# Optimization experiments

Measured on AMD Instinct MI355X. Metric: run time of the kernel, lower is better.

Reference implementation:

```python
import jax, jax.numpy as jnp
import numpy as np

EMBED = 256
HEADS = 8
LEVELS = 1
POINTS = 4
HEAD_DIM = EMBED // HEADS  # 32
SPATIAL = [(200, 200)]     # static (H, W) per level
BS = 2
NQ = 40000
NV = sum(h * w for h, w in SPATIAL)


def setup_inputs() -> dict:
    key = jax.random.key(0)
    ks = jax.random.split(key, 12)
    s = 0.02
    inp = {
        "query": jax.random.normal(ks[0], (BS, NQ, EMBED), jnp.float32),
        "value": jax.random.normal(ks[1], (BS, NV, EMBED), jnp.float32),
        "reference_points": jax.random.uniform(ks[2], (BS, NQ, LEVELS, 2), jnp.float32),
        "spatial_shapes": jnp.array(SPATIAL, dtype=jnp.int32),
        "W_value": jax.random.normal(ks[3], (EMBED, EMBED), jnp.float32) * s,
        "b_value": jax.random.normal(ks[4], (EMBED,), jnp.float32) * s,
        "W_off": jax.random.normal(ks[5], (EMBED, HEADS * LEVELS * POINTS * 2), jnp.float32) * s,
        "b_off": jax.random.normal(ks[6], (HEADS * LEVELS * POINTS * 2,), jnp.float32) * s,
        "W_attn": jax.random.normal(ks[7], (EMBED, HEADS * LEVELS * POINTS), jnp.float32) * s,
        "b_attn": jax.random.normal(ks[8], (HEADS * LEVELS * POINTS,), jnp.float32) * s,
        "W_out": jax.random.normal(ks[9], (EMBED, EMBED), jnp.float32) * s,
        "b_out": jax.random.normal(ks[10], (EMBED,), jnp.float32) * s,
    }
    return inp


def _bilinear_sample(v_l, x, y, H, W):
    """grid_sample(bilinear, padding zeros, align_corners=False) on flat spatial.
    v_l: [bs, heads, H*W, d]; x, y: [bs, nq, heads, P] pixel coords.
    Returns [bs, nq, heads, P, d]."""
    bs = v_l.shape[0]
    nq = x.shape[1]
    x0 = jnp.floor(x)
    y0 = jnp.floor(y)
    out = jnp.zeros((bs, nq, HEADS, POINTS, HEAD_DIM), v_l.dtype)
    for dx in (0, 1):
        for dy in (0, 1):
            xi = x0 + dx
            yi = y0 + dy
            w = (1.0 - jnp.abs(x - xi)) * (1.0 - jnp.abs(y - yi))
            valid = (xi >= 0) & (xi <= W - 1) & (yi >= 0) & (yi <= H - 1)
            xi_c = jnp.clip(xi, 0, W - 1).astype(jnp.int32)
            yi_c = jnp.clip(yi, 0, H - 1).astype(jnp.int32)
            idx = yi_c * W + xi_c                               # [bs,nq,heads,P]
            idx = idx.transpose(0, 2, 1, 3).reshape(bs, HEADS, nq * POINTS)
            g = jnp.take_along_axis(v_l, idx[..., None], axis=2)  # [bs,heads,nq*P,d]
            g = g.reshape(bs, HEADS, nq, POINTS, HEAD_DIM).transpose(0, 2, 1, 3, 4)
            out = out + g * (w * valid.astype(w.dtype))[..., None]
    return out


def reference(query, value, reference_points, spatial_shapes,
              W_value, b_value, W_off, b_off, W_attn, b_attn, W_out, b_out):
    bs, nq, _ = query.shape
    # value projection
    v = (value @ W_value + b_value).reshape(bs, -1, HEADS, HEAD_DIM)
    v = v.transpose(0, 2, 1, 3)  # [bs, heads, nv, d]
    # sampling offsets and attention weights from query
    off = (query @ W_off + b_off).reshape(bs, nq, HEADS, LEVELS, POINTS, 2)
    aw = (query @ W_attn + b_attn).reshape(bs, nq, HEADS, LEVELS * POINTS)
    aw = jax.nn.softmax(aw, axis=-1).reshape(bs, nq, HEADS, LEVELS, POINTS)
    # sampling locations in [0,1] (reference_points last dim == 2 branch)
    normalizer = jnp.stack([spatial_shapes[:, 1], spatial_shapes[:, 0]], -1).astype(query.dtype)  # [L,2]=(W,H)
    loc = reference_points[:, :, None, :, None, :] + off / normalizer[None, None, None, :, None, :]
    out = jnp.zeros((bs, nq, HEADS, HEAD_DIM), query.dtype)
    start = 0
    for lvl, (H, W) in enumerate(SPATIAL):
        v_l = v[:, :, start:start + H * W]            # [bs,heads,HW,d]
        g = 2.0 * loc[:, :, :, lvl] - 1.0             # [bs,nq,heads,P,2] in [-1,1]
        px = ((g[..., 0] + 1.0) * W - 1.0) / 2.0      # align_corners=False
        py = ((g[..., 1] + 1.0) * H - 1.0) / 2.0
        sampled = _bilinear_sample(v_l, px, py, H, W)  # [bs,nq,heads,P,d]
        out = out + (sampled * aw[:, :, :, lvl, :, None]).sum(axis=3)
        start += H * W
    out = out.reshape(bs, nq, EMBED) @ W_out + b_out
    # dropout is identity in eval; identity residual = query (no query_pos)
    return out + query
```

## Files before the change

### kernel.cpp

```cpp
#include <hip/hip_runtime.h>


typedef float  f4  __attribute__((ext_vector_type(4)));
typedef float  fx4 __attribute__((ext_vector_type(4)));
typedef short  s8  __attribute__((ext_vector_type(8)));
typedef short  s4  __attribute__((ext_vector_type(4)));
typedef int    i4  __attribute__((ext_vector_type(4)));
typedef unsigned int u4 __attribute__((ext_vector_type(4)));

#define KDIM    256
#define NVPIX   40000
#define GH      200
#define GW      200
#define LDP     68

__device__ __forceinline__ short f2bf(float f) {
  union { float f; unsigned u; } v; v.f = f;
  unsigned r = v.u + 0x7fffu + ((v.u >> 16) & 1u);
  return (short)(r >> 16);
}
__device__ __forceinline__ float bf2f(unsigned short h) {
  union { unsigned u; float f; } v; v.u = ((unsigned)h) << 16; return v.f;
}
__device__ __forceinline__ float asf(unsigned u) {
  union { unsigned u; float f; } v; v.u = u; return v.f;
}

__global__ void prep_k(const float* __restrict__ Wv, const float* __restrict__ Wo,
                       const float* __restrict__ Woff, const float* __restrict__ Wattn,
                       const float* __restrict__ boff, const float* __restrict__ battn,
                       unsigned short* __restrict__ Wv_t, unsigned short* __restrict__ Wo_t,
                       unsigned short* __restrict__ Wp_t, float* __restrict__ bp)
{
  int i = blockIdx.x * 256 + threadIdx.x;
  if (i < 65536) {
    int n = i >> 8, k = i & 255;
    Wv_t[i] = (unsigned short)f2bf(Wv[k * 256 + n]);
  } else if (i < 131072) {
    int j = i - 65536; int n = j >> 8, k = j & 255;
    Wo_t[j] = (unsigned short)f2bf(Wo[k * 256 + n]);
  } else if (i < 163840) {
    int j = i - 131072; int n = j >> 8, k = j & 255;
    float val = (n < 64) ? Woff[k * 64 + n] : ((n < 96) ? Wattn[k * 32 + (n - 64)] : 0.f);
    Wp_t[j] = (unsigned short)f2bf(val);
  } else if (i < 163968) {
    int j = i - 163840;
    bp[j] = (j < 64) ? boff[j] : ((j < 96) ? battn[j - 64] : 0.f);
  }
}

template<int ABF, int CBF, int RES, int BN>
__global__ __launch_bounds__(512)
void gemm_k(const void* __restrict__ Ap, const unsigned short* __restrict__ Bt,
            const float* __restrict__ bias, const float* __restrict__ resid,
            void* __restrict__ Cp)
{
  constexpr int ACCJ = BN / 64;
  constexpr int WN   = BN / 4;
  __shared__ short As[128 * LDP];
  __shared__ short Bs[BN * LDP];
  const int t  = threadIdx.x;
  const int m0 = blockIdx.x * 128;
  const int lane = t & 63;
  const int w  = t >> 6;
  const int wm = (w >> 2) * 64;
  const int wn = (w & 3) * WN;
  const int fr = lane & 15;
  const int quad = lane >> 4;

  fx4 acc[4][ACCJ];
  #pragma unroll
  for (int i = 0; i < 4; i++)
    #pragma unroll
    for (int j = 0; j < ACCJ; j++) { fx4 z = {0.f, 0.f, 0.f, 0.f}; acc[i][j] = z; }

  f4 pa[4];
  s8 pa8[2];
  s8 pb[ACCJ];

  auto loadA = [&](int k0) {
    if (ABF) {
      const unsigned short* base = (const unsigned short*)Ap + (size_t)m0 * KDIM + k0;
      #pragma unroll
      for (int j = 0; j < 2; j++) {
        int id = t + j * 512;
        int row = id >> 3, kp = (id & 7) * 8;
        pa8[j] = *(const s8*)(base + (size_t)row * KDIM + kp);
      }
    } else {
      const float* base = (const float*)Ap + (size_t)m0 * KDIM + k0;
      #pragma unroll
      for (int j = 0; j < 4; j++) {
        int id = t + j * 512;
        int row = id >> 4, kp = (id & 15) * 4;
        pa[j] = *(const f4*)(base + (size_t)row * KDIM + kp);
      }
    }
  };
  auto loadB = [&](int k0) {
    const unsigned short* base = Bt + k0;
    #pragma unroll
    for (int j = 0; j < ACCJ; j++) {
      int id = t + j * 512;
      int row = id >> 3, kp = (id & 7) * 8;
      pb[j] = *(const s8*)(base + (size_t)row * KDIM + kp);
    }
  };
  auto storeAB = [&]() {
    if (ABF) {
      #pragma unroll
      for (int j = 0; j < 2; j++) {
        int id = t + j * 512;
        int row = id >> 3, kp = (id & 7) * 8;
        *(s8*)(&As[row * LDP + kp]) = pa8[j];
      }
    } else {
      #pragma unroll
      for (int j = 0; j < 4; j++) {
        int id = t + j * 512;
        int row = id >> 4, kp = (id & 15) * 4;
        s4 c;
        #pragma unroll
        for (int e = 0; e < 4; e++) c[e] = f2bf(pa[j][e]);
        *(s4*)(&As[row * LDP + kp]) = c;
      }
    }
    #pragma unroll
    for (int j = 0; j < ACCJ; j++) {
      int id = t + j * 512;
      int row = id >> 3, kp = (id & 7) * 8;
      *(s8*)(&Bs[row * LDP + kp]) = pb[j];
    }
  };

  loadA(0); loadB(0);
  #pragma unroll
  for (int it = 0; it < 4; ++it) {
    __syncthreads();
    storeAB();
    __syncthreads();
    if (it < 3) { loadA((it + 1) * 64); loadB((it + 1) * 64); }
    #pragma unroll
    for (int kk = 0; kk < 2; kk++) {
      s8 afr[4], bfr[ACCJ];
      #pragma unroll
      for (int i = 0; i < 4; i++)
        afr[i] = *(const s8*)(&As[(wm + i * 16 + fr) * LDP + kk * 32 + quad * 8]);
      #pragma unroll
      for (int j = 0; j < ACCJ; j++)
        bfr[j] = *(const s8*)(&Bs[(wn + j * 16 + fr) * LDP + kk * 32 + quad * 8]);
      #pragma unroll
      for (int i = 0; i < 4; i++)
        #pragma unroll
        for (int j = 0; j < ACCJ; j++)
          acc[i][j] = __builtin_amdgcn_mfma_f32_16x16x32_bf16(afr[i], bfr[j], acc[i][j], 0, 0, 0);
    }
  }

  #pragma unroll
  for (int i = 0; i < 4; i++) {
    const int mbase = m0 + wm + i * 16 + quad * 4;
    #pragma unroll
    for (int j = 0; j < ACCJ; j++) {
      const int n = wn + j * 16 + fr;
      const float bn = bias[n];
      #pragma unroll
      for (int r = 0; r < 4; r++) {
        const size_t m = (size_t)(mbase + r);
        float v = acc[i][j][r] + bn;
        if (RES) v += resid[m * (size_t)BN + n];
        if (CBF) ((unsigned short*)Cp)[m * (size_t)BN + n] = (unsigned short)f2bf(v);
        else     ((float*)Cp)[m * (size_t)BN + n] = v;
      }
    }
  }
}

__global__ __launch_bounds__(256, 4)
void sample_k(const unsigned short* __restrict__ v, const float* __restrict__ p,
              const float* __restrict__ ref, unsigned short* __restrict__ o)
{
  const int t  = threadIdx.x;
  const int q0 = blockIdx.x * 8;
  __shared__ float sp[8][128];
  __shared__ float sref[16];
  __shared__ float sw[8][8][4][4];
  __shared__ int   so[8][8][4][4];
  {
    const float* pb = p + (size_t)q0 * 128;
    float* spf = &sp[0][0];
    *(f4*)(spf + t * 4) = *(const f4*)(pb + t * 4);
    if (t < 16) sref[t] = ref[(size_t)q0 * 2 + t];
  }
  __syncthreads();

  {
    const int qa = t >> 5;
    const int ha = (t >> 2) & 7;
    const int pa_ = t & 3;
    const float lg0 = sp[qa][64 + ha * 4 + 0], lg1 = sp[qa][64 + ha * 4 + 1];
    const float lg2 = sp[qa][64 + ha * 4 + 2], lg3 = sp[qa][64 + ha * 4 + 3];
    const float mx = fmaxf(fmaxf(lg0, lg1), fmaxf(lg2, lg3));
    const float e0 = __expf(lg0 - mx), e1 = __expf(lg1 - mx);
    const float e2 = __expf(lg2 - mx), e3 = __expf(lg3 - mx);
    const float inv = 1.f / (e0 + e1 + e2 + e3);
    const float a = ((pa_ == 0) ? e0 : (pa_ == 1) ? e1 : (pa_ == 2) ? e2 : e3) * inv;
    const float rx = sref[qa * 2], ry = sref[qa * 2 + 1];
    const float ox = sp[qa][ha * 8 + pa_ * 2], oy = sp[qa][ha * 8 + pa_ * 2 + 1];
    const float px = rx * 200.f + ox - 0.5f;
    const float py = ry * 200.f + oy - 0.5f;
    const float x0f = floorf(px), y0f = floorf(py);
    const int ix = (int)x0f, iy = (int)y0f;
    const float fx = px - x0f, fy = py - y0f;
    const float vx0 = (ix >= 0 && ix < GW) ? 1.f : 0.f;
    const float vx1 = (ix + 1 >= 0 && ix + 1 < GW) ? 1.f : 0.f;
    const float vy0 = (iy >= 0 && iy < GH) ? 1.f : 0.f;
    const float vy1 = (iy + 1 >= 0 && iy + 1 < GH) ? 1.f : 0.f;
    f4 wv;
    wv[0] = a * (1.f - fx) * (1.f - fy) * vx0 * vy0;
    wv[1] = a * fx * (1.f - fy) * vx1 * vy0;
    wv[2] = a * (1.f - fx) * fy * vx0 * vy1;
    wv[3] = a * fx * fy * vx1 * vy1;
    const int ix0c = min(max(ix, 0), GW - 1);
    const int ix1c = min(max(ix + 1, 0), GW - 1);
    const int iy0c = min(max(iy, 0), GH - 1);
    const int iy1c = min(max(iy + 1, 0), GH - 1);
    const int r0 = iy0c * (GW * 256);
    const int r1 = iy1c * (GW * 256);
    i4 ov;
    ov[0] = r0 + ix0c * 256;
    ov[1] = r0 + ix1c * 256;
    ov[2] = r1 + ix0c * 256;
    ov[3] = r1 + ix1c * 256;
    *(f4*)&sw[qa][ha][pa_][0] = wv;
    *(i4*)&so[qa][ha][pa_][0] = ov;
  }
  __syncthreads();

  const int qi = t >> 5;
  const int h  = (t >> 2) & 7;
  const int dg = t & 3;
  const int q  = q0 + qi;
  const unsigned short* vb = v + ((q0 >= 40000) ? (size_t)NVPIX * 256 : 0);
  const int cbase = h * 32 + dg * 8;

  i4 ofs[4];
  #pragma unroll
  for (int pt = 0; pt < 4; pt++) ofs[pt] = *(const i4*)&so[qi][h][pt][0];

  u4 g[16];
  #pragma unroll
  for (int pt = 0; pt < 4; pt++)
    #pragma unroll
    for (int c = 0; c < 4; c++)
      g[pt * 4 + c] = *(const u4*)(vb + (unsigned)(ofs[pt][c] + cbase));

  f4 wts[4];
  #pragma unroll
  for (int pt = 0; pt < 4; pt++) wts[pt] = *(const f4*)&sw[qi][h][pt][0];

  float acc[8];
  #pragma unroll
  for (int e = 0; e < 8; e++) acc[e] = 0.f;

  #pragma unroll
  for (int pt = 0; pt < 4; pt++) {
    #pragma unroll
    for (int c = 0; c < 4; c++) {
      const float wk = wts[pt][c];
      const u4 gu = g[pt * 4 + c];
      #pragma unroll
      for (int d = 0; d < 4; d++) {
        const unsigned u = gu[d];
        acc[2 * d]     += wk * asf(u << 16);
        acc[2 * d + 1] += wk * asf(u & 0xffff0000u);
      }
    }
  }

  s8 res;
  #pragma unroll
  for (int e = 0; e < 8; e++) res[e] = f2bf(acc[e]);
  *(s8*)(o + (size_t)q * 256 + cbase) = res;
}

extern "C" void kernel_launch(void* const* d_in, const int* in_sizes, int n_in,
                              void* d_out, int out_size, void* d_ws, size_t ws_size,
                              hipStream_t stream)
{
  const float* query = (const float*)d_in[0];
  const float* value = (const float*)d_in[1];
  const float* refp  = (const float*)d_in[2];
  const float* Wv    = (const float*)d_in[4];
  const float* bv    = (const float*)d_in[5];
  const float* Woff  = (const float*)d_in[6];
  const float* boff  = (const float*)d_in[7];
  const float* Wattn = (const float*)d_in[8];
  const float* battn = (const float*)d_in[9];
  const float* Wo    = (const float*)d_in[10];
  const float* bo    = (const float*)d_in[11];

  char* ws = (char*)d_ws;
  unsigned short* ws_v = (unsigned short*)ws;
  float*          ws_p = (float*)(ws + 40960000);
  unsigned short* ws_o = (unsigned short*)(ws + 81920000);
  unsigned short* Wv_t = (unsigned short*)(ws + 122880000);
  unsigned short* Wo_t = Wv_t + 65536;
  unsigned short* Wp_t = Wo_t + 65536;
  float*          bp   = (float*)(Wp_t + 32768);

  hipLaunchKernelGGL(prep_k, dim3(641), dim3(256), 0, stream,
                     Wv, Wo, Woff, Wattn, boff, battn, Wv_t, Wo_t, Wp_t, bp);
  hipLaunchKernelGGL((gemm_k<0, 1, 0, 256>), dim3(625), dim3(512), 0, stream,
                     (const void*)value, Wv_t, bv, (const float*)nullptr, (void*)ws_v);
  hipLaunchKernelGGL((gemm_k<0, 0, 0, 128>), dim3(625), dim3(512), 0, stream,
                     (const void*)query, Wp_t, bp, (const float*)nullptr, (void*)ws_p);
  hipLaunchKernelGGL(sample_k, dim3(10000), dim3(256), 0, stream,
                     ws_v, ws_p, refp, ws_o);
  hipLaunchKernelGGL((gemm_k<1, 0, 1, 256>), dim3(625), dim3(512), 0, stream,
                     (const void*)ws_o, Wo_t, bo, query, (void*)d_out);
}
```

Baseline: 341.4 us.

## Double-buffer GEMM shared tiles with two-deep register prefetch and lighter barriers

Measured after the change: 328.6 us. 3.7% less time.

```diff
diff --git a/kernel.cpp b/kernel.cpp
--- a/kernel.cpp
+++ b/kernel.cpp
@@ -57,8 +57,8 @@
 {
   constexpr int ACCJ = BN / 64;
   constexpr int WN   = BN / 4;
-  __shared__ short As[128 * LDP];
-  __shared__ short Bs[BN * LDP];
+  __shared__ short As[2][128 * LDP];
+  __shared__ short Bs[2][BN * LDP];
   const int t  = threadIdx.x;
   const int m0 = blockIdx.x * 128;
   const int lane = t & 63;
@@ -74,88 +74,94 @@
     #pragma unroll
     for (int j = 0; j < ACCJ; j++) { fx4 z = {0.f, 0.f, 0.f, 0.f}; acc[i][j] = z; }
 
-  f4 pa[4];
-  s8 pa8[2];
-  s8 pb[ACCJ];
-
-  auto loadA = [&](int k0) {
+  f4 paf[2][4];
+  s8 pab[2][2];
+  s8 pb [2][ACCJ];
+
+  auto loadT = [&](int k0, int s) {
     if (ABF) {
       const unsigned short* base = (const unsigned short*)Ap + (size_t)m0 * KDIM + k0;
       #pragma unroll
       for (int j = 0; j < 2; j++) {
         int id = t + j * 512;
-        int row = id >> 3, kp = (id & 7) * 8;
-        pa8[j] = *(const s8*)(base + (size_t)row * KDIM + kp);
+        pab[s][j] = *(const s8*)(base + (size_t)(id >> 3) * KDIM + (id & 7) * 8);
       }
     } else {
       const float* base = (const float*)Ap + (size_t)m0 * KDIM + k0;
       #pragma unroll
       for (int j = 0; j < 4; j++) {
         int id = t + j * 512;
-        int row = id >> 4, kp = (id & 15) * 4;
-        pa[j] = *(const f4*)(base + (size_t)row * KDIM + kp);
-      }
-    }
-  };
-  auto loadB = [&](int k0) {
-    const unsigned short* base = Bt + k0;
+        paf[s][j] = *(const f4*)(base + (size_t)(id >> 4) * KDIM + (id & 15) * 4);
+      }
+    }
+    const unsigned short* bbase = Bt + k0;
     #pragma unroll
     for (int j = 0; j < ACCJ; j++) {
       int id = t + j * 512;
-      int row = id >> 3, kp = (id & 7) * 8;
-      pb[j] = *(const s8*)(base + (size_t)row * KDIM + kp);
+      pb[s][j] = *(const s8*)(bbase + (size_t)(id >> 3) * KDIM + (id & 7) * 8);
     }
   };
-  auto storeAB = [&]() {
+  auto storeT = [&](int buf, int s) {
     if (ABF) {
       #pragma unroll
       for (int j = 0; j < 2; j++) {
         int id = t + j * 512;
-        int row = id >> 3, kp = (id & 7) * 8;
-        *(s8*)(&As[row * LDP + kp]) = pa8[j];
+        *(s8*)(&As[buf][(id >> 3) * LDP + (id & 7) * 8]) = pab[s][j];
       }
     } else {
       #pragma unroll
       for (int j = 0; j < 4; j++) {
         int id = t + j * 512;
-        int row = id >> 4, kp = (id & 15) * 4;
         s4 c;
         #pragma unroll
-        for (int e = 0; e < 4; e++) c[e] = f2bf(pa[j][e]);
-        *(s4*)(&As[row * LDP + kp]) = c;
+        for (int e = 0; e < 4; e++) c[e] = f2bf(paf[s][j][e]);
+        *(s4*)(&As[buf][(id >> 4) * LDP + (id & 15) * 4]) = c;
       }
     }
     #pragma unroll
     for (int j = 0; j < ACCJ; j++) {
       int id = t + j * 512;
-      int row = id >> 3, kp = (id & 7) * 8;
-      *(s8*)(&Bs[row * LDP + kp]) = pb[j];
+      *(s8*)(&Bs[buf][(id >> 3) * LDP + (id & 7) * 8]) = pb[s][j];
     }
   };
-
-  loadA(0); loadB(0);
-  #pragma unroll
-  for (int it = 0; it < 4; ++it) {
-    __syncthreads();
-    storeAB();
-    __syncthreads();
-    if (it < 3) { loadA((it + 1) * 64); loadB((it + 1) * 64); }
+  auto compute = [&](int buf) {
     #pragma unroll
     for (int kk = 0; kk < 2; kk++) {
       s8 afr[4], bfr[ACCJ];
       #pragma unroll
       for (int i = 0; i < 4; i++)
-        afr[i] = *(const s8*)(&As[(wm + i * 16 + fr) * LDP + kk * 32 + quad * 8]);
+        afr[i] = *(const s8*)(&As[buf][(wm + i * 16 + fr) * LDP + kk * 32 + quad * 8]);
       #pragma unroll
       for (int j = 0; j < ACCJ; j++)
-        bfr[j] = *(const s8*)(&Bs[(wn + j * 16 + fr) * LDP + kk * 32 + quad * 8]);
+        bfr[j] = *(const s8*)(&Bs[buf][(wn + j * 16 + fr) * LDP + kk * 32 + quad * 8]);
       #pragma unroll
       for (int i = 0; i < 4; i++)
         #pragma unroll
         for (int j = 0; j < ACCJ; j++)
           acc[i][j] = __builtin_amdgcn_mfma_f32_16x16x32_bf16(afr[i], bfr[j], acc[i][j], 0, 0, 0);
     }
-  }
+  };
+
+#define GBAR() do { asm volatile("s_waitcnt lgkmcnt(0)" ::: "memory"); \
+                    __builtin_amdgcn_s_barrier(); } while (0)
+
+  loadT(0, 0);
+  loadT(64, 1);
+  storeT(0, 0);
+  GBAR();
+  loadT(128, 0);
+  compute(0);
+  storeT(1, 1);
+  GBAR();
+  loadT(192, 1);
+  compute(1);
+  storeT(0, 0);
+  GBAR();
+  compute(0);
+  storeT(1, 1);
+  GBAR();
+  compute(1);
+#undef GBAR
 
   #pragma unroll
   for (int i = 0; i < 4; i++) {
@@ -255,6 +261,8 @@
     for (int c = 0; c < 4; c++)
       g[pt * 4 + c] = *(const u4*)(vb + (unsigned)(ofs[pt][c] + cbase));
 
+  __builtin_amdgcn_sched_barrier(0);
+
   f4 wts[4];
   #pragma unroll
   for (int pt = 0; pt < 4; pt++) wts[pt] = *(const f4*)&sw[qi][h][pt][0];
```

## Merge value and projection GEMMs into one launch with 128x128 tiles

Applied to the files above, without the earlier changes.

Result: slower. 425.0 us (+24.5%).

```diff
diff --git a/kernel.cpp b/kernel.cpp
--- a/kernel.cpp
+++ b/kernel.cpp
@@ -49,59 +49,55 @@
   }
 }
 
-template<int ABF, int CBF, int RES, int BN>
-__global__ __launch_bounds__(512)
-void gemm_k(const void* __restrict__ Ap, const unsigned short* __restrict__ Bt,
-            const float* __restrict__ bias, const float* __restrict__ resid,
-            void* __restrict__ Cp)
-{
-  constexpr int ACCJ = BN / 64;
-  constexpr int WN   = BN / 4;
-  __shared__ short As[128 * LDP];
-  __shared__ short Bs[BN * LDP];
+template<int ABF, int CBF, int RES>
+__device__ __forceinline__
+void gemm_body(const void* __restrict__ Ap, const unsigned short* __restrict__ Bt,
+               const float* __restrict__ bias, const float* __restrict__ resid,
+               void* __restrict__ Cp, int N, int m0, int n0,
+               short* __restrict__ As, short* __restrict__ Bs)
+{
   const int t  = threadIdx.x;
-  const int m0 = blockIdx.x * 128;
   const int lane = t & 63;
   const int w  = t >> 6;
-  const int wm = (w >> 2) * 64;
-  const int wn = (w & 3) * WN;
+  const int wm = (w >> 1) * 64;
+  const int wn = (w & 1) * 64;
   const int fr = lane & 15;
   const int quad = lane >> 4;
 
-  fx4 acc[4][ACCJ];
+  fx4 acc[4][4];
   #pragma unroll
   for (int i = 0; i < 4; i++)
     #pragma unroll
-    for (int j = 0; j < ACCJ; j++) { fx4 z = {0.f, 0.f, 0.f, 0.f}; acc[i][j] = z; }
-
-  f4 pa[4];
-  s8 pa8[2];
-  s8 pb[ACCJ];
+    for (int j = 0; j < 4; j++) { fx4 z = {0.f, 0.f, 0.f, 0.f}; acc[i][j] = z; }
+
+  f4 pa[8];
+  s8 pa8[4];
+  s8 pb[4];
 
   auto loadA = [&](int k0) {
     if (ABF) {
       const unsigned short* base = (const unsigned short*)Ap + (size_t)m0 * KDIM + k0;
       #pragma unroll
-      for (int j = 0; j < 2; j++) {
-        int id = t + j * 512;
+      for (int j = 0; j < 4; j++) {
+        int id = t + j * 256;
         int row = id >> 3, kp = (id & 7) * 8;
         pa8[j] = *(const s8*)(base + (size_t)row * KDIM + kp);
       }
     } else {
       const float* base = (const float*)Ap + (size_t)m0 * KDIM + k0;
       #pragma unroll
-      for (int j = 0; j < 4; j++) {
-        int id = t + j * 512;
+      for (int j = 0; j < 8; j++) {
+        int id = t + j * 256;
         int row = id >> 4, kp = (id & 15) * 4;
         pa[j] = *(const f4*)(base + (size_t)row * KDIM + kp);
       }
     }
   };
   auto loadB = [&](int k0) {
-    const unsigned short* base = Bt + k0;
-    #pragma unroll
-    for (int j = 0; j < ACCJ; j++) {
-      int id = t + j * 512;
+    const unsigned short* base = Bt + (size_t)n0 * KDIM + k0;
+    #pragma unroll
+    for (int j = 0; j < 4; j++) {
+      int id = t + j * 256;
       int row = id >> 3, kp = (id & 7) * 8;
       pb[j] = *(const s8*)(base + (size_t)row * KDIM + kp);
     }
@@ -109,15 +105,15 @@
   auto storeAB = [&]() {
     if (ABF) {
       #pragma unroll
-      for (int j = 0; j < 2; j++) {
-        int id = t + j * 512;
+      for (int j = 0; j < 4; j++) {
+        int id = t + j * 256;
         int row = id >> 3, kp = (id & 7) * 8;
         *(s8*)(&As[row * LDP + kp]) = pa8[j];
       }
     } else {
       #pragma unroll
-      for (int j = 0; j < 4; j++) {
-        int id = t + j * 512;
+      for (int j = 0; j < 8; j++) {
+        int id = t + j * 256;
         int row = id >> 4, kp = (id & 15) * 4;
         s4 c;
         #pragma unroll
@@ -126,8 +122,8 @@
       }
     }
     #pragma unroll
-    for (int j = 0; j < ACCJ; j++) {
-      int id = t + j * 512;
+    for (int j = 0; j < 4; j++) {
+      int id = t + j * 256;
       int row = id >> 3, kp = (id & 7) * 8;
       *(s8*)(&Bs[row * LDP + kp]) = pb[j];
     }
@@ -142,17 +138,17 @@
     if (it < 3) { loadA((it + 1) * 64); loadB((it + 1) * 64); }
     #pragma unroll
     for (int kk = 0; kk < 2; kk++) {
-      s8 afr[4], bfr[ACCJ];
+      s8 afr[4], bfr[4];
       #pragma unroll
       for (int i = 0; i < 4; i++)
         afr[i] = *(const s8*)(&As[(wm + i * 16 + fr) * LDP + kk * 32 + quad * 8]);
       #pragma unroll
-      for (int j = 0; j < ACCJ; j++)
-        bfr[j] = *(const s8*)(&Bs[(wn + j * 16 + fr) * LDP + kk * 32 + quad * 8]);
+      for (int i = 0; i < 4; i++)
+        bfr[i] = *(const s8*)(&Bs[(wn + i * 16 + fr) * LDP + kk * 32 + quad * 8]);
       #pragma unroll
       for (int i = 0; i < 4; i++)
         #pragma unroll
-        for (int j = 0; j < ACCJ; j++)
+        for (int j = 0; j < 4; j++)
           acc[i][j] = __builtin_amdgcn_mfma_f32_16x16x32_bf16(afr[i], bfr[j], acc[i][j], 0, 0, 0);
     }
   }
@@ -161,19 +157,48 @@
   for (int i = 0; i < 4; i++) {
     const int mbase = m0 + wm + i * 16 + quad * 4;
     #pragma unroll
-    for (int j = 0; j < ACCJ; j++) {
-      const int n = wn + j * 16 + fr;
+    for (int j = 0; j < 4; j++) {
+      const int n = n0 + wn + j * 16 + fr;
       const float bn = bias[n];
       #pragma unroll
       for (int r = 0; r < 4; r++) {
         const size_t m = (size_t)(mbase + r);
         float v = acc[i][j][r] + bn;
-        if (RES) v += resid[m * (size_t)BN + n];
-        if (CBF) ((unsigned short*)Cp)[m * (size_t)BN + n] = (unsigned short)f2bf(v);
-        else     ((float*)Cp)[m * (size_t)BN + n] = v;
-      }
-    }
-  }
+        if (RES) v += resid[m * (size_t)N + n];
+        if (CBF) ((unsigned short*)Cp)[m * (size_t)N + n] = (unsigned short)f2bf(v);
+        else     ((float*)Cp)[m * (size_t)N + n] = v;
+      }
+    }
+  }
+}
+
+__global__ __launch_bounds__(256)
+void fused_vp_k(const float* __restrict__ value, const unsigned short* __restrict__ Wv_t,
+                const float* __restrict__ bv, unsigned short* __restrict__ ws_v,
+                const float* __restrict__ query, const unsigned short* __restrict__ Wp_t,
+                const float* __restrict__ bp, float* __restrict__ ws_p)
+{
+  __shared__ short As[128 * LDP];
+  __shared__ short Bs[128 * LDP];
+  const int m0 = blockIdx.x * 128;
+  if (blockIdx.y == 2) {
+    gemm_body<0, 0, 0>((const void*)query, Wp_t, bp, nullptr, (void*)ws_p,
+                       128, m0, 0, As, Bs);
+  } else {
+    gemm_body<0, 1, 0>((const void*)value, Wv_t, bv, nullptr, (void*)ws_v,
+                       256, m0, blockIdx.y * 128, As, Bs);
+  }
+}
+
+__global__ __launch_bounds__(256)
+void gemm_out_k(const unsigned short* __restrict__ samp, const unsigned short* __restrict__ Wo_t,
+                const float* __restrict__ bo, const float* __restrict__ query,
+                float* __restrict__ out)
+{
+  __shared__ short As[128 * LDP];
+  __shared__ short Bs[128 * LDP];
+  gemm_body<1, 0, 1>((const void*)samp, Wo_t, bo, query, (void*)out,
+                     256, blockIdx.x * 128, blockIdx.y * 128, As, Bs);
 }
 
 __global__ __launch_bounds__(256, 4)
@@ -255,6 +280,8 @@
     for (int c = 0; c < 4; c++)
       g[pt * 4 + c] = *(const u4*)(vb + (unsigned)(ofs[pt][c] + cbase));
 
+  __builtin_amdgcn_sched_barrier(0);
+
   f4 wts[4];
   #pragma unroll
   for (int pt = 0; pt < 4; pt++) wts[pt] = *(const f4*)&sw[qi][h][pt][0];
@@ -311,12 +338,10 @@
 
   hipLaunchKernelGGL(prep_k, dim3(641), dim3(256), 0, stream,
                      Wv, Wo, Woff, Wattn, boff, battn, Wv_t, Wo_t, Wp_t, bp);
-  hipLaunchKernelGGL((gemm_k<0, 1, 0, 256>), dim3(625), dim3(512), 0, stream,
-                     (const void*)value, Wv_t, bv, (const float*)nullptr, (void*)ws_v);
-  hipLaunchKernelGGL((gemm_k<0, 0, 0, 128>), dim3(625), dim3(512), 0, stream,
-                     (const void*)query, Wp_t, bp, (const float*)nullptr, (void*)ws_p);
+  hipLaunchKernelGGL(fused_vp_k, dim3(625, 3), dim3(256), 0, stream,
+                     value, Wv_t, bv, ws_v, query, Wp_t, bp, ws_p);
   hipLaunchKernelGGL(sample_k, dim3(10000), dim3(256), 0, stream,
                      ws_v, ws_p, refp, ws_o);
-  hipLaunchKernelGGL((gemm_k<1, 0, 1, 256>), dim3(625), dim3(512), 0, stream,
-                     (const void*)ws_o, Wo_t, bo, query, (void*)d_out);
-}
+  hipLaunchKernelGGL(gemm_out_k, dim3(625, 2), dim3(256), 0, stream,
+                     ws_o, Wo_t, bo, query, (float*)d_out);
+}
```
